# Performance work log

Hardware: AMD Instinct MI355X
Metric: run time of the kernel (lower is better)

Reference implementation:

```python
import jax, jax.numpy as jnp
import numpy as np

N_RAYS = 65536
N_PTS = 128
EPS = 1e-10
FAR_DELTA = 1e10  # sentinel delta for last sample, as in the torch module


def setup_inputs() -> dict:
    key = jax.random.key(0)
    k1, k2, k3 = jax.random.split(key, 3)
    # ray sample depths must be increasing along the sample axis
    depth_values = jnp.sort(jax.random.uniform(k1, (N_RAYS, N_PTS)) * 6.0 + 0.1, axis=-1)
    density = jax.random.uniform(k2, (N_RAYS, N_PTS, 1)) * 2.0  # non-negative densities
    feature = jax.random.uniform(k3, (N_RAYS, N_PTS, 3))        # rgb features in [0,1)
    return {"depth_values": depth_values, "density": density, "feature": feature}


def reference(depth_values, density, feature):
    # deltas: successive depth differences, huge value for the last sample  [N, P, 1]
    deltas = jnp.concatenate(
        [depth_values[:, 1:] - depth_values[:, :-1],
         jnp.full_like(depth_values[:, :1], FAR_DELTA)], axis=-1)[..., None]

    # transmittance: exclusive cumulative product of exp(-density*(delta+eps)),
    # computed as exp of an exclusive cumsum in log space (fused scan, no python loop)
    s = density[:, :, 0] * (deltas[:, :, 0] + EPS)            # [N, P]
    log_trans = -jnp.cumsum(s, axis=1)
    log_trans = jnp.concatenate(
        [jnp.zeros_like(log_trans[:, :1]), log_trans[:, :-1]], axis=1)
    trans = jnp.exp(log_trans)[..., None]                      # [N, P, 1]

    # alpha-weights, faithful to torch: trans * (1 - exp(-density*deltas + eps))
    weights = trans * (1.0 - jnp.exp(-density * deltas + EPS))  # [N, P, 1]

    # aggregate rgb feature  [N, 3]
    feat_out = jnp.sum(weights * feature, axis=1)

    # depth normalized by global max, then aggregated  [N, 1]
    depth_norm = depth_values / jnp.max(depth_values)
    depth_out = jnp.sum(weights * depth_norm[..., None], axis=1)

    return feat_out, depth_out
```

## Files before the change

kernel.cpp:

```cpp
#include <hip/hip_runtime.h>

#define N_PTS 128
#define FAR_DELTA 1e10f
#define EPS 1e-10f
#define RPB 8

__global__ __launch_bounds__(256) void vr_main(
    const float* __restrict__ depth,
    const float* __restrict__ density,
    const float* __restrict__ feature,
    float* __restrict__ feat_out,
    float* __restrict__ depth_out,
    float* __restrict__ blk_max,
    int n_rays)
{
    __shared__ float bmax[RPB];

    const int t   = threadIdx.x;
    const int q   = t >> 5;
    const int sl  = t & 31;
    const int ray = blockIdx.x * RPB + q;

    const float4* dp4 = (const float4*)(depth   + (size_t)ray * N_PTS);
    const float4* rp4 = (const float4*)(density + (size_t)ray * N_PTS);
    const float4* fp4 = (const float4*)(feature + (size_t)ray * N_PTS * 3);

    float4 d4 = dp4[sl];
    float4 r4 = rp4[sl];
    float4 f0 = fp4[sl * 3 + 0];
    float4 f1 = fp4[sl * 3 + 1];
    float4 f2 = fp4[sl * 3 + 2];

    if (sl == 31) bmax[q] = d4.w;

    float nd = __shfl_down(d4.x, 1, 32);
    float delta0 = d4.y - d4.x;
    float delta1 = d4.z - d4.y;
    float delta2 = d4.w - d4.z;
    float delta3 = (sl == 31) ? FAR_DELTA : (nd - d4.w);

    float s0 = r4.x * (delta0 + EPS);
    float s1 = r4.y * (delta1 + EPS);
    float s2 = r4.z * (delta2 + EPS);
    float s3 = r4.w * (delta3 + EPS);

    float p1 = s0;
    float p2 = s0 + s1;
    float p3 = p2 + s2;
    float tt = p3 + ((sl == 31) ? 0.0f : s3);

    float inc = tt;
    #pragma unroll
    for (int off = 1; off < 32; off <<= 1) {
        float n = __shfl_up(inc, off, 32);
        if (sl >= off) inc += n;
    }
    float excl = inc - tt;

    float w0 = __expf(-excl)        * (1.0f - __expf(fmaf(-r4.x, delta0, EPS)));
    float w1 = __expf(-(excl + p1)) * (1.0f - __expf(fmaf(-r4.y, delta1, EPS)));
    float w2 = __expf(-(excl + p2)) * (1.0f - __expf(fmaf(-r4.z, delta2, EPS)));
    float w3 = __expf(-(excl + p3)) * (1.0f - __expf(fmaf(-r4.w, delta3, EPS)));

    float acc0 = w0 * f0.x + w1 * f0.w + w2 * f1.z + w3 * f2.y;
    float acc1 = w0 * f0.y + w1 * f1.x + w2 * f1.w + w3 * f2.z;
    float acc2 = w0 * f0.z + w1 * f1.y + w2 * f2.x + w3 * f2.w;
    float accd = w0 * d4.x + w1 * d4.y + w2 * d4.z + w3 * d4.w;

    #pragma unroll
    for (int off = 16; off > 0; off >>= 1) {
        acc0 += __shfl_xor(acc0, off, 32);
        acc1 += __shfl_xor(acc1, off, 32);
        acc2 += __shfl_xor(acc2, off, 32);
        accd += __shfl_xor(accd, off, 32);
    }

    if (sl == 0 && ray < n_rays) {
        float* fo = feat_out + (size_t)ray * 3;
        fo[0] = acc0;
        fo[1] = acc1;
        fo[2] = acc2;
        depth_out[ray] = accd;
    }

    __syncthreads();
    if (t == 0) {
        float m = bmax[0];
        #pragma unroll
        for (int i = 1; i < RPB; ++i) m = fmaxf(m, bmax[i]);
        blk_max[blockIdx.x] = m;
    }
}

__global__ __launch_bounds__(256) void vr_epilogue(
    const float* __restrict__ blk_max, float* __restrict__ depth_out,
    int nb, int n_rays)
{
    const int t = threadIdx.x;

    float m = 0.0f;
    for (int i = t; i < nb; i += 256) m = fmaxf(m, blk_max[i]);
    #pragma unroll
    for (int off = 32; off > 0; off >>= 1)
        m = fmaxf(m, __shfl_xor(m, off, 64));

    __shared__ float wm[4];
    if ((t & 63) == 0) wm[t >> 6] = m;
    __syncthreads();
    float gm = fmaxf(fmaxf(wm[0], wm[1]), fmaxf(wm[2], wm[3]));

    int i = blockIdx.x * 256 + t;
    if (i < n_rays) depth_out[i] *= (1.0f / gm);
}

extern "C" void kernel_launch(void* const* d_in, const int* in_sizes, int n_in,
                              void* d_out, int out_size, void* d_ws, size_t ws_size,
                              hipStream_t stream)
{
    const float* depth   = (const float*)d_in[0];
    const float* density = (const float*)d_in[1];
    const float* feature = (const float*)d_in[2];

    const int n_rays = in_sizes[0] / N_PTS;

    float* out       = (float*)d_out;
    float* feat_out  = out;
    float* depth_out = out + (size_t)n_rays * 3;
    float* blk_max   = (float*)d_ws;

    const int nb = n_rays / RPB;

    vr_main<<<nb, 256, 0, stream>>>(depth, density, feature,
                                    feat_out, depth_out, blk_max, n_rays);

    const int eb = (n_rays + 255) / 256;
    vr_epilogue<<<eb, 256, 0, stream>>>(blk_max, depth_out, nb, n_rays);
}
```

Measured before the change: 37.29 us.

## Use 16 lanes per ray with 8 samples each and per-wave max

Each ray is now handled by 16 lanes that each process 8 consecutive samples, so a block covers 16 rays. This shortens the shuffle scan and the reductions, and gives each thread more independent loads and exps. The per-block shared-memory max and __syncthreads are replaced by a cross-lane shuffle max written per wave. The epilogue then has to reduce four times as many partial maxima, and each thread holds more registers.

```diff
diff --git a/kernel.cpp b/kernel.cpp
--- a/kernel.cpp
+++ b/kernel.cpp
@@ -3,7 +3,7 @@
 #define N_PTS 128
 #define FAR_DELTA 1e10f
 #define EPS 1e-10f
-#define RPB 8
+#define RPB 16
 
 __global__ __launch_bounds__(256) void vr_main(
     const float* __restrict__ depth,
@@ -11,95 +11,103 @@
     const float* __restrict__ feature,
     float* __restrict__ feat_out,
     float* __restrict__ depth_out,
-    float* __restrict__ blk_max,
+    float* __restrict__ wave_max,
     int n_rays)
 {
-    __shared__ float bmax[RPB];
+    const int t   = threadIdx.x;
+    const int sl  = t & 15;
+    const int ray = (blockIdx.x * 256 + t) >> 4;
 
-    const int t   = threadIdx.x;
-    const int q   = t >> 5;
-    const int sl  = t & 31;
-    const int ray = blockIdx.x * RPB + q;
+    const float4* dp4 = (const float4*)(depth   + (size_t)ray * N_PTS) + 2 * sl;
+    const float4* rp4 = (const float4*)(density + (size_t)ray * N_PTS) + 2 * sl;
+    const float4* fp4 = (const float4*)(feature + (size_t)ray * N_PTS * 3) + 6 * sl;
 
-    const float4* dp4 = (const float4*)(depth   + (size_t)ray * N_PTS);
-    const float4* rp4 = (const float4*)(density + (size_t)ray * N_PTS);
-    const float4* fp4 = (const float4*)(feature + (size_t)ray * N_PTS * 3);
+    float4 dA = dp4[0], dB = dp4[1];
+    float4 rA = rp4[0], rB = rp4[1];
+    float4 f0 = fp4[0], f1 = fp4[1], f2 = fp4[2];
+    float4 f3 = fp4[3], f4 = fp4[4], f5 = fp4[5];
 
-    float4 d4 = dp4[sl];
-    float4 r4 = rp4[sl];
-    float4 f0 = fp4[sl * 3 + 0];
-    float4 f1 = fp4[sl * 3 + 1];
-    float4 f2 = fp4[sl * 3 + 2];
+    float nd = __shfl_down(dA.x, 1, 16);
+    float dl0 = dA.y - dA.x;
+    float dl1 = dA.z - dA.y;
+    float dl2 = dA.w - dA.z;
+    float dl3 = dB.x - dA.w;
+    float dl4 = dB.y - dB.x;
+    float dl5 = dB.z - dB.y;
+    float dl6 = dB.w - dB.z;
+    float dl7 = (sl == 15) ? FAR_DELTA : (nd - dB.w);
 
-    if (sl == 31) bmax[q] = d4.w;
+    float s0 = rA.x * (dl0 + EPS);
+    float s1 = rA.y * (dl1 + EPS);
+    float s2 = rA.z * (dl2 + EPS);
+    float s3 = rA.w * (dl3 + EPS);
+    float s4 = rB.x * (dl4 + EPS);
+    float s5 = rB.y * (dl5 + EPS);
+    float s6 = rB.z * (dl6 + EPS);
+    float s7 = rB.w * (dl7 + EPS);
 
-    float nd = __shfl_down(d4.x, 1, 32);
-    float delta0 = d4.y - d4.x;
-    float delta1 = d4.z - d4.y;
-    float delta2 = d4.w - d4.z;
-    float delta3 = (sl == 31) ? FAR_DELTA : (nd - d4.w);
+    float P1 = s0;
+    float P2 = P1 + s1;
+    float P3 = P2 + s2;
+    float P4 = P3 + s3;
+    float P5 = P4 + s4;
+    float P6 = P5 + s5;
+    float P7 = P6 + s6;
+    float T  = P7 + ((sl == 15) ? 0.0f : s7);
 
-    float s0 = r4.x * (delta0 + EPS);
-    float s1 = r4.y * (delta1 + EPS);
-    float s2 = r4.z * (delta2 + EPS);
-    float s3 = r4.w * (delta3 + EPS);
-
-    float p1 = s0;
-    float p2 = s0 + s1;
-    float p3 = p2 + s2;
-    float tt = p3 + ((sl == 31) ? 0.0f : s3);
-
-    float inc = tt;
+    float inc = T;
     #pragma unroll
-    for (int off = 1; off < 32; off <<= 1) {
-        float n = __shfl_up(inc, off, 32);
+    for (int off = 1; off < 16; off <<= 1) {
+        float n = __shfl_up(inc, off, 16);
         if (sl >= off) inc += n;
     }
-    float excl = inc - tt;
+    float ex = inc - T;
 
-    float w0 = __expf(-excl)        * (1.0f - __expf(fmaf(-r4.x, delta0, EPS)));
-    float w1 = __expf(-(excl + p1)) * (1.0f - __expf(fmaf(-r4.y, delta1, EPS)));
-    float w2 = __expf(-(excl + p2)) * (1.0f - __expf(fmaf(-r4.z, delta2, EPS)));
-    float w3 = __expf(-(excl + p3)) * (1.0f - __expf(fmaf(-r4.w, delta3, EPS)));
+    float w0 = __expf(-ex)        * (1.0f - __expf(fmaf(-rA.x, dl0, EPS)));
+    float w1 = __expf(-(ex + P1)) * (1.0f - __expf(fmaf(-rA.y, dl1, EPS)));
+    float w2 = __expf(-(ex + P2)) * (1.0f - __expf(fmaf(-rA.z, dl2, EPS)));
+    float w3 = __expf(-(ex + P3)) * (1.0f - __expf(fmaf(-rA.w, dl3, EPS)));
+    float w4 = __expf(-(ex + P4)) * (1.0f - __expf(fmaf(-rB.x, dl4, EPS)));
+    float w5 = __expf(-(ex + P5)) * (1.0f - __expf(fmaf(-rB.y, dl5, EPS)));
+    float w6 = __expf(-(ex + P6)) * (1.0f - __expf(fmaf(-rB.z, dl6, EPS)));
+    float w7 = __expf(-(ex + P7)) * (1.0f - __expf(fmaf(-rB.w, dl7, EPS)));
 
-    float acc0 = w0 * f0.x + w1 * f0.w + w2 * f1.z + w3 * f2.y;
-    float acc1 = w0 * f0.y + w1 * f1.x + w2 * f1.w + w3 * f2.z;
-    float acc2 = w0 * f0.z + w1 * f1.y + w2 * f2.x + w3 * f2.w;
-    float accd = w0 * d4.x + w1 * d4.y + w2 * d4.z + w3 * d4.w;
+    float a0 = w0*f0.x + w1*f0.w + w2*f1.z + w3*f2.y + w4*f3.x + w5*f3.w + w6*f4.z + w7*f5.y;
+    float a1 = w0*f0.y + w1*f1.x + w2*f1.w + w3*f2.z + w4*f3.y + w5*f4.x + w6*f4.w + w7*f5.z;
+    float a2 = w0*f0.z + w1*f1.y + w2*f2.x + w3*f2.w + w4*f3.z + w5*f4.y + w6*f5.x + w7*f5.w;
+    float ad = w0*dA.x + w1*dA.y + w2*dA.z + w3*dA.w + w4*dB.x + w5*dB.y + w6*dB.z + w7*dB.w;
 
     #pragma unroll
-    for (int off = 16; off > 0; off >>= 1) {
-        acc0 += __shfl_xor(acc0, off, 32);
-        acc1 += __shfl_xor(acc1, off, 32);
-        acc2 += __shfl_xor(acc2, off, 32);
-        accd += __shfl_xor(accd, off, 32);
+    for (int off = 8; off > 0; off >>= 1) {
+        a0 += __shfl_xor(a0, off, 16);
+        a1 += __shfl_xor(a1, off, 16);
+        a2 += __shfl_xor(a2, off, 16);
+        ad += __shfl_xor(ad, off, 16);
     }
 
-    if (sl == 0 && ray < n_rays) {
+    if (sl == 0) {
         float* fo = feat_out + (size_t)ray * 3;
-        fo[0] = acc0;
-        fo[1] = acc1;
-        fo[2] = acc2;
-        depth_out[ray] = accd;
+        fo[0] = a0;
+        fo[1] = a1;
+        fo[2] = a2;
+        depth_out[ray] = ad;
     }
 
-    __syncthreads();
-    if (t == 0) {
-        float m = bmax[0];
-        #pragma unroll
-        for (int i = 1; i < RPB; ++i) m = fmaxf(m, bmax[i]);
-        blk_max[blockIdx.x] = m;
-    }
+    float cand = (sl == 15) ? dB.w : 0.0f;
+    cand = fmaxf(cand, __shfl_xor(cand, 16, 64));
+    cand = fmaxf(cand, __shfl_xor(cand, 32, 64));
+    if ((t & 63) == 15)
+        wave_max[(blockIdx.x * 256 + t) >> 6] = cand;
 }
 
 __global__ __launch_bounds__(256) void vr_epilogue(
-    const float* __restrict__ blk_max, float* __restrict__ depth_out,
-    int nb, int n_rays)
+    const float* __restrict__ wave_max, float* __restrict__ depth_out,
+    int nw, int n_rays)
 {
     const int t = threadIdx.x;
 
     float m = 0.0f;
-    for (int i = t; i < nb; i += 256) m = fmaxf(m, blk_max[i]);
+    for (int i = t; i < nw; i += 256) m = fmaxf(m, wave_max[i]);
     #pragma unroll
     for (int off = 32; off > 0; off >>= 1)
         m = fmaxf(m, __shfl_xor(m, off, 64));
@@ -126,13 +134,14 @@
     float* out       = (float*)d_out;
     float* feat_out  = out;
     float* depth_out = out + (size_t)n_rays * 3;
-    float* blk_max   = (float*)d_ws;
+    float* wave_max  = (float*)d_ws;
 
-    const int nb = n_rays / RPB;
+    const int nb_main = n_rays / RPB;
+    const int nw      = n_rays / 4;
 
-    vr_main<<<nb, 256, 0, stream>>>(depth, density, feature,
-                                    feat_out, depth_out, blk_max, n_rays);
+    vr_main<<<nb_main, 256, 0, stream>>>(depth, density, feature,
+                                         feat_out, depth_out, wave_max, n_rays);
 
     const int eb = (n_rays + 255) / 256;
-    vr_epilogue<<<eb, 256, 0, stream>>>(blk_max, depth_out, nb, n_rays);
+    vr_epilogue<<<eb, 256, 0, stream>>>(wave_max, depth_out, nw, n_rays);
 }
```

After: 41.47 us. 11.2% more time.

## Use persistent grid-stride blocks and shrink the per-block max reduction

Applied to the files above, without the earlier changes.

The main kernel now launches a fixed 2048 blocks. Each block loops over 4 ray tiles and keeps a running depth maximum, so blk_max holds 2048 entries instead of 8192. The epilogue reads those 2048 partial maxima with two float4 loads per thread instead of a strided loop over 8192. This cuts the redundant global-max work that every epilogue block repeats. The risk is less memory-level parallelism in the main kernel, since each wave handles its tiles serially with an unroll-1 loop.

```diff
diff --git a/kernel.cpp b/kernel.cpp
--- a/kernel.cpp
+++ b/kernel.cpp
@@ -3,7 +3,9 @@
 #define N_PTS 128
 #define FAR_DELTA 1e10f
 #define EPS 1e-10f
-#define RPB 8
+#define RPT 8
+#define NBLK 2048
+#define TPB 4
 
 __global__ __launch_bounds__(256) void vr_main(
     const float* __restrict__ depth,
@@ -14,92 +16,104 @@
     float* __restrict__ blk_max,
     int n_rays)
 {
-    __shared__ float bmax[RPB];
+    __shared__ float wmax[4];
 
-    const int t   = threadIdx.x;
-    const int q   = t >> 5;
-    const int sl  = t & 31;
-    const int ray = blockIdx.x * RPB + q;
+    const int t  = threadIdx.x;
+    const int q  = t >> 5;
+    const int sl = t & 31;
 
-    const float4* dp4 = (const float4*)(depth   + (size_t)ray * N_PTS);
-    const float4* rp4 = (const float4*)(density + (size_t)ray * N_PTS);
-    const float4* fp4 = (const float4*)(feature + (size_t)ray * N_PTS * 3);
+    const int n_tiles = n_rays / RPT;
+    float rmax = 0.0f;
 
-    float4 d4 = dp4[sl];
-    float4 r4 = rp4[sl];
-    float4 f0 = fp4[sl * 3 + 0];
-    float4 f1 = fp4[sl * 3 + 1];
-    float4 f2 = fp4[sl * 3 + 2];
+    #pragma unroll 1
+    for (int it = 0; it < TPB; ++it) {
+        const int tile = it * NBLK + blockIdx.x;
+        if (tile >= n_tiles) break;
+        const int ray = tile * RPT + q;
 
-    if (sl == 31) bmax[q] = d4.w;
+        const float4* dp4 = (const float4*)(depth   + (size_t)ray * N_PTS);
+        const float4* rp4 = (const float4*)(density + (size_t)ray * N_PTS);
+        const float4* fp4 = (const float4*)(feature + (size_t)ray * N_PTS * 3);
 
-    float nd = __shfl_down(d4.x, 1, 32);
-    float delta0 = d4.y - d4.x;
-    float delta1 = d4.z - d4.y;
-    float delta2 = d4.w - d4.z;
-    float delta3 = (sl == 31) ? FAR_DELTA : (nd - d4.w);
+        float4 d4 = dp4[sl];
+        float4 r4 = rp4[sl];
+        float4 f0 = fp4[sl * 3 + 0];
+        float4 f1 = fp4[sl * 3 + 1];
+        float4 f2 = fp4[sl * 3 + 2];
 
-    float s0 = r4.x * (delta0 + EPS);
-    float s1 = r4.y * (delta1 + EPS);
-    float s2 = r4.z * (delta2 + EPS);
-    float s3 = r4.w * (delta3 + EPS);
+        float nd = __shfl_down(d4.x, 1, 32);
+        float delta0 = d4.y - d4.x;
+        float delta1 = d4.z - d4.y;
+        float delta2 = d4.w - d4.z;
+        float delta3 = (sl == 31) ? FAR_DELTA : (nd - d4.w);
 
-    float p1 = s0;
-    float p2 = s0 + s1;
-    float p3 = p2 + s2;
-    float tt = p3 + ((sl == 31) ? 0.0f : s3);
+        float s0 = r4.x * (delta0 + EPS);
+        float s1 = r4.y * (delta1 + EPS);
+        float s2 = r4.z * (delta2 + EPS);
+        float s3 = r4.w * (delta3 + EPS);
 
-    float inc = tt;
-    #pragma unroll
-    for (int off = 1; off < 32; off <<= 1) {
-        float n = __shfl_up(inc, off, 32);
-        if (sl >= off) inc += n;
-    }
-    float excl = inc - tt;
+        float p1 = s0;
+        float p2 = s0 + s1;
+        float p3 = p2 + s2;
+        float tt = p3 + ((sl == 31) ? 0.0f : s3);
 
-    float w0 = __expf(-excl)        * (1.0f - __expf(fmaf(-r4.x, delta0, EPS)));
-    float w1 = __expf(-(excl + p1)) * (1.0f - __expf(fmaf(-r4.y, delta1, EPS)));
-    float w2 = __expf(-(excl + p2)) * (1.0f - __expf(fmaf(-r4.z, delta2, EPS)));
-    float w3 = __expf(-(excl + p3)) * (1.0f - __expf(fmaf(-r4.w, delta3, EPS)));
+        float inc = tt;
+        #pragma unroll
+        for (int off = 1; off < 32; off <<= 1) {
+            float n = __shfl_up(inc, off, 32);
+            if (sl >= off) inc += n;
+        }
+        float excl = inc - tt;
 
-    float acc0 = w0 * f0.x + w1 * f0.w + w2 * f1.z + w3 * f2.y;
-    float acc1 = w0 * f0.y + w1 * f1.x + w2 * f1.w + w3 * f2.z;
-    float acc2 = w0 * f0.z + w1 * f1.y + w2 * f2.x + w3 * f2.w;
-    float accd = w0 * d4.x + w1 * d4.y + w2 * d4.z + w3 * d4.w;
+        float w0 = __expf(-excl)        * (1.0f - __expf(fmaf(-r4.x, delta0, EPS)));
+        float w1 = __expf(-(excl + p1)) * (1.0f - __expf(fmaf(-r4.y, delta1, EPS)));
+        float w2 = __expf(-(excl + p2)) * (1.0f - __expf(fmaf(-r4.z, delta2, EPS)));
+        float w3 = __expf(-(excl + p3)) * (1.0f - __expf(fmaf(-r4.w, delta3, EPS)));
 
-    #pragma unroll
-    for (int off = 16; off > 0; off >>= 1) {
-        acc0 += __shfl_xor(acc0, off, 32);
-        acc1 += __shfl_xor(acc1, off, 32);
-        acc2 += __shfl_xor(acc2, off, 32);
-        accd += __shfl_xor(accd, off, 32);
+        float acc0 = w0 * f0.x + w1 * f0.w + w2 * f1.z + w3 * f2.y;
+        float acc1 = w0 * f0.y + w1 * f1.x + w2 * f1.w + w3 * f2.z;
+        float acc2 = w0 * f0.z + w1 * f1.y + w2 * f2.x + w3 * f2.w;
+        float accd = w0 * d4.x + w1 * d4.y + w2 * d4.z + w3 * d4.w;
+
+        #pragma unroll
+        for (int off = 16; off > 0; off >>= 1) {
+            acc0 += __shfl_xor(acc0, off, 32);
+            acc1 += __shfl_xor(acc1, off, 32);
+            acc2 += __shfl_xor(acc2, off, 32);
+            accd += __shfl_xor(accd, off, 32);
+        }
+
+        if (sl == 0) {
+            float* fo = feat_out + (size_t)ray * 3;
+            fo[0] = acc0;
+            fo[1] = acc1;
+            fo[2] = acc2;
+            depth_out[ray] = accd;
+        }
+
+        rmax = fmaxf(rmax, d4.w);
     }
 
-    if (sl == 0 && ray < n_rays) {
-        float* fo = feat_out + (size_t)ray * 3;
-        fo[0] = acc0;
-        fo[1] = acc1;
-        fo[2] = acc2;
-        depth_out[ray] = accd;
-    }
-
+    float other = __shfl_xor(rmax, 32, 64);
+    if (t == (q & ~1) * 32 + 31) {}
+    if ((t & 63) == 31) wmax[t >> 6] = fmaxf(rmax, other);
     __syncthreads();
-    if (t == 0) {
-        float m = bmax[0];
-        #pragma unroll
-        for (int i = 1; i < RPB; ++i) m = fmaxf(m, bmax[i]);
-        blk_max[blockIdx.x] = m;
-    }
+    if (t == 0)
+        blk_max[blockIdx.x] = fmaxf(fmaxf(wmax[0], wmax[1]),
+                                    fmaxf(wmax[2], wmax[3]));
 }
 
 __global__ __launch_bounds__(256) void vr_epilogue(
     const float* __restrict__ blk_max, float* __restrict__ depth_out,
-    int nb, int n_rays)
+    int n_rays)
 {
     const int t = threadIdx.x;
 
-    float m = 0.0f;
-    for (int i = t; i < nb; i += 256) m = fmaxf(m, blk_max[i]);
+    const float4* bm4 = (const float4*)blk_max;
+    float4 a = bm4[t];
+    float4 b = bm4[t + 256];
+    float m = fmaxf(fmaxf(fmaxf(a.x, a.y), fmaxf(a.z, a.w)),
+                    fmaxf(fmaxf(b.x, b.y), fmaxf(b.z, b.w)));
     #pragma unroll
     for (int off = 32; off > 0; off >>= 1)
         m = fmaxf(m, __shfl_xor(m, off, 64));
@@ -128,11 +142,9 @@
     float* depth_out = out + (size_t)n_rays * 3;
     float* blk_max   = (float*)d_ws;
 
-    const int nb = n_rays / RPB;
-
-    vr_main<<<nb, 256, 0, stream>>>(depth, density, feature,
-                                    feat_out, depth_out, blk_max, n_rays);
+    vr_main<<<NBLK, 256, 0, stream>>>(depth, density, feature,
+                                      feat_out, depth_out, blk_max, n_rays);
 
     const int eb = (n_rays + 255) / 256;
-    vr_epilogue<<<eb, 256, 0, stream>>>(blk_max, depth_out, nb, n_rays);
+    vr_epilogue<<<eb, 256, 0, stream>>>(blk_max, depth_out, n_rays);
 }
```

After: 33.46 us. -10.3%, faster.
